# Performance work log

Hardware: AMD Instinct MI355X
Metric: run time of the kernel (lower is better)

The kernel has to match this reference:

```python
import jax, jax.numpy as jnp
import numpy as np

H = 5120       # hidden_size
NH = 128       # num_heads
QLR = 1536     # q_lora_rank
DR = 64        # qk_rope_head_dim
KVLR = 512     # kv_lora_rank
DV = 128       # v_head_dim
DN = 128       # qk_nope_head_dim
DQ = 192       # q_head_dim
THETA = 10000.0
EPS = 1e-6


def _rmsnorm(x, w, eps=EPS):
    xf = x.astype(jnp.float32)
    var = jnp.mean(xf * xf, axis=-1, keepdims=True)
    return (w * (xf * jax.lax.rsqrt(var + eps))).astype(x.dtype)


def _rope(x, cos, sin):
    # Llama-style complex rotation on interleaved pairs along last dim.
    xr = x.reshape(x.shape[:-1] + (-1, 2))
    x0, x1 = xr[..., 0], xr[..., 1]
    out = jnp.stack([x0 * cos - x1 * sin, x0 * sin + x1 * cos], axis=-1)
    return out.reshape(x.shape)


def setup_inputs() -> dict:
    key = jax.random.key(0)
    ks = jax.random.split(key, 8)
    b, kv_len = 2, 2048
    s = 0.02  # scaled-down normal init for numerical sanity (math unchanged)
    return {
        "hidden_states": jax.random.normal(ks[0], (b, 1, H), jnp.float32),
        "compressed_kv_normed_cache": jax.random.normal(ks[1], (b, kv_len, KVLR), jnp.float32),
        "k_pe_cache": jax.random.normal(ks[2], (b, kv_len, DR), jnp.float32),
        "q_a_w": jax.random.normal(ks[3], (QLR, H), jnp.float32) * s,
        "q_a_ln_w": jnp.ones((QLR,), jnp.float32),
        "q_b_w": jax.random.normal(ks[4], (NH * DQ, QLR), jnp.float32) * s,
        "kv_b_w": jax.random.normal(ks[5], (NH * (DN + DV), KVLR), jnp.float32) * s,
        "o_w": jax.random.normal(ks[6], (H, NH * DV), jnp.float32) * s,
    }


def reference(hidden_states, compressed_kv_normed_cache, k_pe_cache,
              q_a_w, q_a_ln_w, q_b_w, kv_b_w, o_w):
    b = hidden_states.shape[0]
    kv_len = k_pe_cache.shape[1]

    # Q path: down-proj -> RMSNorm -> up-proj
    q_a = jnp.einsum('bqh,rh->bqr', hidden_states, q_a_w)          # [b,1,QLR]
    q_a = _rmsnorm(q_a, q_a_ln_w)
    q = jnp.einsum('bqr,or->bqo', q_a, q_b_w).reshape(b, NH, DQ)   # q_len==1
    q_nope, q_pe = q[..., :DN], q[..., DN:]                        # [b,NH,128],[b,NH,64]

    # RoPE tables
    inv_freq = 1.0 / (THETA ** (jnp.arange(0, DR, 2, dtype=jnp.float32) / DR))  # [32]
    ang = jnp.arange(kv_len, dtype=jnp.float32)[:, None] * inv_freq             # [kv_len,32]
    cos, sin = jnp.cos(ang), jnp.sin(ang)

    # query rotated at position kv_len-1 (torch code repeats q then takes last slot)
    q_pe = _rope(q_pe, cos[-1], sin[-1])                           # [b,NH,64]
    k_pe = _rope(k_pe_cache, cos[None], sin[None])                 # [b,kv_len,64]

    # KV decompression (shared latent -> per-head nope-key and value)
    kv = jnp.einsum('bkc,oc->bko', compressed_kv_normed_cache, kv_b_w)
    kv = kv.reshape(b, kv_len, NH, DN + DV)
    k_nope, v = kv[..., :DN], kv[..., DN:]                         # [b,kv,NH,128] each

    # scores: nope part + rope part (k_pe broadcast across heads)
    scores = (jnp.einsum('bhd,bkhd->bhk', q_nope, k_nope)
              + jnp.einsum('bhd,bkd->bhk', q_pe, k_pe)) * (DQ ** -0.5)
    attn = jax.nn.softmax(scores.astype(jnp.float32), axis=-1).astype(hidden_states.dtype)

    out = jnp.einsum('bhk,bkhd->bhd', attn, v).reshape(b, 1, NH * DV)
    return jnp.einsum('bqo,ho->bqh', out, o_w)                     # [b,1,H]
```

## Files before the change

kernel.cpp:

```cpp
#include <hip/hip_runtime.h>
#include <math.h>

constexpr int kH    = 5120;
constexpr int kQLR  = 1536;
constexpr int kNH   = 128;
constexpr int kDQ   = 192;
constexpr int kDN   = 128;
constexpr int kDR   = 64;
constexpr int kKVLR = 512;
constexpr int kDV   = 128;

template<int IN, int SPLIT, bool ATOMIC>
__global__ __launch_bounds__(256) void gemv2_k(const float* __restrict__ W,
                                               const float* __restrict__ x,
                                               float* __restrict__ y, int R) {
  constexpr int CH = IN / SPLIT;
  constexpr int F4 = CH / 256;
  int lane = threadIdx.x & 63, wave = threadIdx.x >> 6;
  int r0 = blockIdx.x * 8 + wave * 2;
  int c0 = blockIdx.y * CH;
  const float4* W0 = (const float4*)(W + (size_t)r0 * IN + c0);
  const float4* W1 = (const float4*)(W + (size_t)(r0 + 1) * IN + c0);
  const float4* x0 = (const float4*)(x + c0);
  const float4* x1 = (const float4*)(x + IN + c0);
  float a00 = 0.f, a01 = 0.f, a10 = 0.f, a11 = 0.f;
#pragma unroll 4
  for (int i = 0; i < F4; ++i) {
    int idx = lane + (i << 6);
    float4 w0 = W0[idx];
    float4 w1 = W1[idx];
    float4 u = x0[idx];
    float4 v = x1[idx];
    a00 = fmaf(w0.x,u.x,fmaf(w0.y,u.y,fmaf(w0.z,u.z,fmaf(w0.w,u.w,a00))));
    a01 = fmaf(w0.x,v.x,fmaf(w0.y,v.y,fmaf(w0.z,v.z,fmaf(w0.w,v.w,a01))));
    a10 = fmaf(w1.x,u.x,fmaf(w1.y,u.y,fmaf(w1.z,u.z,fmaf(w1.w,u.w,a10))));
    a11 = fmaf(w1.x,v.x,fmaf(w1.y,v.y,fmaf(w1.z,v.z,fmaf(w1.w,v.w,a11))));
  }
#pragma unroll
  for (int off = 32; off > 0; off >>= 1) {
    a00 += __shfl_down(a00, off, 64);
    a01 += __shfl_down(a01, off, 64);
    a10 += __shfl_down(a10, off, 64);
    a11 += __shfl_down(a11, off, 64);
  }
  if (lane == 0) {
    if (ATOMIC) {
      atomicAdd(&y[r0], a00);
      atomicAdd(&y[(size_t)R + r0], a01);
      atomicAdd(&y[r0 + 1], a10);
      atomicAdd(&y[(size_t)R + r0 + 1], a11);
    } else {
      y[r0] = a00;
      y[(size_t)R + r0] = a01;
      y[r0 + 1] = a10;
      y[(size_t)R + r0 + 1] = a11;
    }
  }
}

__global__ __launch_bounds__(256) void rmsnorm_k(const float* __restrict__ qa,
                                                 const float* __restrict__ w,
                                                 float* __restrict__ out) {
  int b = blockIdx.x, t = threadIdx.x;
  const float* x = qa + (size_t)b * kQLR;
  float s = 0.f;
  for (int i = t; i < kQLR; i += 256) { float v = x[i]; s = fmaf(v, v, s); }
  __shared__ float red[4];
#pragma unroll
  for (int off = 32; off > 0; off >>= 1) s += __shfl_down(s, off, 64);
  if ((t & 63) == 0) red[t >> 6] = s;
  __syncthreads();
  float tot = red[0] + red[1] + red[2] + red[3];
  float scale = rsqrtf(tot / (float)kQLR + 1e-6f);
  for (int i = t; i < kQLR; i += 256) out[(size_t)b * kQLR + i] = x[i] * scale * w[i];
}

__global__ __launch_bounds__(256) void qabs_k(const float* __restrict__ q,
                                              const float* __restrict__ kvw,
                                              float* __restrict__ qabs) {
  int h = blockIdx.x, ds = blockIdx.y;
  int t = threadIdx.x;
  __shared__ float qn[2][32];
  if (t < 64) {
    int b = t >> 5, d = t & 31;
    qn[b][d] = q[((size_t)b * kNH + h) * kDQ + ds * 32 + d];
  }
  __syncthreads();
  float a0x = 0.f, a0y = 0.f, a1x = 0.f, a1y = 0.f;
  const float* wb = kvw + ((size_t)h * 256 + ds * 32) * kKVLR + t * 2;
#pragma unroll 4
  for (int d = 0; d < 32; ++d) {
    float2 w = *(const float2*)(wb + (size_t)d * kKVLR);
    float q0 = qn[0][d], q1 = qn[1][d];
    a0x = fmaf(q0, w.x, a0x); a0y = fmaf(q0, w.y, a0y);
    a1x = fmaf(q1, w.x, a1x); a1y = fmaf(q1, w.y, a1y);
  }
  float* p0 = qabs + (size_t)h * kKVLR + t * 2;
  float* p1 = qabs + ((size_t)kNH + h) * kKVLR + t * 2;
  atomicAdd(p0, a0x); atomicAdd(p0 + 1, a0y);
  atomicAdd(p1, a1x); atomicAdd(p1 + 1, a1y);
}

__global__ __launch_bounds__(256) void attn_k(const float* __restrict__ qabs,
                                              const float* __restrict__ qfull,
                                              const float* __restrict__ c,
                                              const float* __restrict__ kpe,
                                              float* __restrict__ ctxp,
                                              float* __restrict__ ml, int KV) {
  int ks = blockIdx.x, hg = blockIdx.y, b = blockIdx.z;
  int t = threadIdx.x, lane = t & 63, wave = t >> 6;
  int h0 = __builtin_amdgcn_readfirstlane(hg * 16 + wave * 4);
  int k0 = ks * 64;
  __shared__ float cl[64 * 129];
  __shared__ float kl[64 * 65];
  __shared__ float ql[16 * 64];
  __shared__ float al[64 * 20];

  constexpr float kNegLog = -0.28782313662425572f;

  {
    const float4* src = (const float4*)(kpe + ((size_t)b * KV + k0) * kDR);
#pragma unroll
    for (int i = 0; i < 4; ++i) {
      int idx = t + i * 256;
      int r = idx >> 4, c4 = idx & 15;
      float4 v = src[r * 16 + c4];
      float fk = (float)(k0 + r);
      float inv0 = expf(kNegLog * (float)(c4 * 2));
      float inv1 = expf(kNegLog * (float)(c4 * 2 + 1));
      float s0, c0, s1, c1;
      sincosf(fk * inv0, &s0, &c0);
      sincosf(fk * inv1, &s1, &c1);
      float* d = &kl[r * 65 + (c4 << 2)];
      d[0] = v.x * c0 - v.y * s0;
      d[1] = v.x * s0 + v.y * c0;
      d[2] = v.z * c1 - v.w * s1;
      d[3] = v.z * s1 + v.w * c1;
    }
  }
  {
    float fp = (float)(KV - 1);
    for (int pi = t; pi < 512; pi += 256) {
      int j = pi >> 5, i = pi & 31;
      float inv = expf(kNegLog * (float)i);
      float s, cc;
      sincosf(fp * inv, &s, &cc);
      const float* qp = qfull + ((size_t)b * kNH + hg * 16 + j) * kDQ + kDN + 2 * i;
      float x0 = qp[0], x1 = qp[1];
      ql[j * 64 + 2 * i]     = x0 * cc - x1 * s;
      ql[j * 64 + 2 * i + 1] = x0 * s + x1 * cc;
    }
  }

  float acc[4] = {0.f, 0.f, 0.f, 0.f};
  for (int cch = 0; cch < 4; ++cch) {
    __syncthreads();
    const float* cb = c + ((size_t)b * KV + k0) * kKVLR + cch * 128;
#pragma unroll
    for (int i = 0; i < 8; ++i) {
      int idx = t + i * 256;
      int r = idx >> 5, c4 = idx & 31;
      float4 v = *(const float4*)(cb + (size_t)r * kKVLR + (c4 << 2));
      float* d = &cl[r * 129 + (c4 << 2)];
      d[0] = v.x; d[1] = v.y; d[2] = v.z; d[3] = v.w;
    }
    __syncthreads();
    const float* qb = qabs + ((size_t)b * kNH + h0) * kKVLR + cch * 128;
#pragma unroll 4
    for (int cc2 = 0; cc2 < 128; ++cc2) {
      float cv = cl[lane * 129 + cc2];
#pragma unroll
      for (int j = 0; j < 4; ++j)
        acc[j] = fmaf(cv, qb[(size_t)j * kKVLR + cc2], acc[j]);
    }
  }
  {
#pragma unroll 4
    for (int i = 0; i < 64; ++i) {
      float kv = kl[lane * 65 + i];
#pragma unroll
      for (int j = 0; j < 4; ++j)
        acc[j] = fmaf(kv, ql[(wave * 4 + j) * 64 + i], acc[j]);
    }
  }

  const float scale = 1.0f / sqrtf(192.0f);
  float pj[4], mj[4], lj[4];
#pragma unroll
  for (int j = 0; j < 4; ++j) {
    float s = acc[j] * scale;
    float m = s;
#pragma unroll
    for (int off = 32; off > 0; off >>= 1) m = fmaxf(m, __shfl_xor(m, off, 64));
    float p = __expf(s - m);
    float l = p;
#pragma unroll
    for (int off = 32; off > 0; off >>= 1) l += __shfl_xor(l, off, 64);
    pj[j] = p; mj[j] = m; lj[j] = l;
  }
  *(float4*)&al[lane * 20 + wave * 4] = make_float4(pj[0], pj[1], pj[2], pj[3]);
  if (lane == 0) {
#pragma unroll
    for (int j = 0; j < 4; ++j) {
      float2* mp = (float2*)(ml + (((size_t)b * kNH + h0 + j) * 32 + ks) * 2);
      *mp = make_float2(mj[j], lj[j]);
    }
  }
  __syncthreads();

  float2 accv[16];
#pragma unroll
  for (int j = 0; j < 16; ++j) accv[j] = make_float2(0.f, 0.f);
  const float2* c2 = (const float2*)(c + ((size_t)b * KV + k0) * kKVLR);
#pragma unroll 2
  for (int k = 0; k < 64; ++k) {
    float2 cv = c2[k * (kKVLR / 2) + t];
#pragma unroll
    for (int j4 = 0; j4 < 4; ++j4) {
      float4 av = *(const float4*)&al[k * 20 + j4 * 4];
      accv[j4*4+0].x = fmaf(av.x, cv.x, accv[j4*4+0].x);
      accv[j4*4+0].y = fmaf(av.x, cv.y, accv[j4*4+0].y);
      accv[j4*4+1].x = fmaf(av.y, cv.x, accv[j4*4+1].x);
      accv[j4*4+1].y = fmaf(av.y, cv.y, accv[j4*4+1].y);
      accv[j4*4+2].x = fmaf(av.z, cv.x, accv[j4*4+2].x);
      accv[j4*4+2].y = fmaf(av.z, cv.y, accv[j4*4+2].y);
      accv[j4*4+3].x = fmaf(av.w, cv.x, accv[j4*4+3].x);
      accv[j4*4+3].y = fmaf(av.w, cv.y, accv[j4*4+3].y);
    }
  }
#pragma unroll
  for (int j = 0; j < 16; ++j) {
    float2* dst = (float2*)(ctxp + (((size_t)ks * 2 + b) * kNH + hg * 16 + j) * kKVLR);
    dst[t] = accv[j];
  }
}

__global__ __launch_bounds__(256) void vproj_k(const float* __restrict__ ctxp,
                                               const float* __restrict__ ml,
                                               const float* __restrict__ kvw,
                                               float* __restrict__ oh) {
  int h = blockIdx.x, dq = blockIdx.y;
  int t = threadIdx.x, lane = t & 63, wave = t >> 6;
  __shared__ float cf[2 * kKVLR];
  __shared__ float invl[2];
  {
    int b = t >> 7, g = t & 127;
    const float2* mlb = (const float2*)(ml + ((size_t)b * kNH + h) * 64);
    float M = -1e30f;
#pragma unroll 8
    for (int s = 0; s < 32; ++s) M = fmaxf(M, mlb[s].x);
    float L = 0.f;
    float4 a4 = make_float4(0.f, 0.f, 0.f, 0.f);
#pragma unroll 4
    for (int s = 0; s < 32; ++s) {
      float2 e = mlb[s];
      float w = __expf(e.x - M);
      L = fmaf(w, e.y, L);
      const float4* p = (const float4*)(ctxp + (((size_t)s * 2 + b) * kNH + h) * kKVLR);
      float4 v = p[g];
      a4.x = fmaf(w, v.x, a4.x);
      a4.y = fmaf(w, v.y, a4.y);
      a4.z = fmaf(w, v.z, a4.z);
      a4.w = fmaf(w, v.w, a4.w);
    }
    *(float4*)&cf[b * kKVLR + (g << 2)] = a4;
    if (g == 0) invl[b] = 1.0f / L;
  }
  __syncthreads();
  float cr0[8], cr1[8];
#pragma unroll
  for (int j = 0; j < 8; ++j) {
    cr0[j] = cf[lane * 8 + j];
    cr1[j] = cf[kKVLR + lane * 8 + j];
  }
#pragma unroll
  for (int i = 0; i < 8; ++i) {
    int d = dq * 32 + wave * 8 + i;
    const float4* w4 = (const float4*)(kvw + ((size_t)h * 256 + 128 + d) * kKVLR) + lane * 2;
    float4 wa = w4[0], wb = w4[1];
    float s0 = wa.x * cr0[0] + wa.y * cr0[1] + wa.z * cr0[2] + wa.w * cr0[3]
             + wb.x * cr0[4] + wb.y * cr0[5] + wb.z * cr0[6] + wb.w * cr0[7];
    float s1 = wa.x * cr1[0] + wa.y * cr1[1] + wa.z * cr1[2] + wa.w * cr1[3]
             + wb.x * cr1[4] + wb.y * cr1[5] + wb.z * cr1[6] + wb.w * cr1[7];
#pragma unroll
    for (int off = 32; off > 0; off >>= 1) {
      s0 += __shfl_down(s0, off, 64);
      s1 += __shfl_down(s1, off, 64);
    }
    if (lane == 0) {
      oh[(size_t)h * kDV + d] = s0 * invl[0];
      oh[((size_t)kNH + h) * kDV + d] = s1 * invl[1];
    }
  }
}

extern "C" void kernel_launch(void* const* d_in, const int* in_sizes, int n_in,
                              void* d_out, int out_size, void* d_ws, size_t ws_size,
                              hipStream_t stream) {
  const float* hs   = (const float*)d_in[0];
  const float* ckv  = (const float*)d_in[1];
  const float* kpe  = (const float*)d_in[2];
  const float* qaw  = (const float*)d_in[3];
  const float* qlnw = (const float*)d_in[4];
  const float* qbw  = (const float*)d_in[5];
  const float* kvbw = (const float*)d_in[6];
  const float* ow   = (const float*)d_in[7];
  float* out = (float*)d_out;

  int B  = in_sizes[0] / kH;
  int KV = in_sizes[2] / (B * kDR);

  float* ws   = (float*)d_ws;
  float* qa   = ws;
  float* qabs = qa + (size_t)B * kQLR;
  float* qan  = qabs + (size_t)B * kNH * kKVLR;
  float* q    = qan + (size_t)B * kQLR;
  float* ctxp = q + (size_t)B * kNH * kDQ;
  float* ml   = ctxp + (size_t)32 * B * kNH * kKVLR;
  float* oh   = ml + (size_t)B * kNH * 64;

  hipMemsetAsync(qa, 0, ((size_t)B * kQLR + (size_t)B * kNH * kKVLR) * sizeof(float), stream);
  hipMemsetAsync(out, 0, (size_t)out_size * sizeof(float), stream);

  gemv2_k<kH, 4, true><<<dim3(kQLR / 8, 4), 256, 0, stream>>>(qaw, hs, qa, kQLR);
  rmsnorm_k<<<B, 256, 0, stream>>>(qa, qlnw, qan);
  gemv2_k<kQLR, 1, false><<<dim3((kNH * kDQ) / 8, 1), 256, 0, stream>>>(qbw, qan, q, kNH * kDQ);
  qabs_k<<<dim3(kNH, 4), 256, 0, stream>>>(q, kvbw, qabs);
  attn_k<<<dim3(KV / 64, 8, B), 256, 0, stream>>>(qabs, q, ckv, kpe, ctxp, ml, KV);
  vproj_k<<<dim3(kNH, 4), 256, 0, stream>>>(ctxp, ml, kvbw, oh);
  gemv2_k<kNH * kDV, 4, true><<<dim3(kH / 8, 4), 256, 0, stream>>>(ow, oh, out, kH);
}
```

Before: 662.0 us.

## Split split-KV fold from vproj and drop atomics in q absorption

The q-absorption kernel now has each block reduce over all 128 nope dims for a column chunk and write directly, replacing four-way split atomics and the large workspace memset. The split-KV softmax merge is moved out of vproj into a separate fold kernel. Before, each of the four dq blocks per head recomputed the same 32-partial reduction over ctxp; now it is done once. This adds one kernel launch and an intermediate ctx buffer. The q-absorption grid also shrinks to fewer, smaller blocks, so less parallelism is available there.

```diff
diff --git a/kernel.cpp b/kernel.cpp
--- a/kernel.cpp
+++ b/kernel.cpp
@@ -75,30 +75,30 @@
   for (int i = t; i < kQLR; i += 256) out[(size_t)b * kQLR + i] = x[i] * scale * w[i];
 }
 
-__global__ __launch_bounds__(256) void qabs_k(const float* __restrict__ q,
-                                              const float* __restrict__ kvw,
-                                              float* __restrict__ qabs) {
-  int h = blockIdx.x, ds = blockIdx.y;
+__global__ __launch_bounds__(128) void qabs2_k(const float* __restrict__ q,
+                                               const float* __restrict__ kvw,
+                                               float* __restrict__ qabs) {
+  int h = blockIdx.x, ch = blockIdx.y;
   int t = threadIdx.x;
-  __shared__ float qn[2][32];
-  if (t < 64) {
-    int b = t >> 5, d = t & 31;
-    qn[b][d] = q[((size_t)b * kNH + h) * kDQ + ds * 32 + d];
+  __shared__ float qn[2][128];
+  for (int i = t; i < 256; i += 128) {
+    int b = i >> 7, d = i & 127;
+    qn[b][d] = q[((size_t)b * kNH + h) * kDQ + d];
   }
   __syncthreads();
   float a0x = 0.f, a0y = 0.f, a1x = 0.f, a1y = 0.f;
-  const float* wb = kvw + ((size_t)h * 256 + ds * 32) * kKVLR + t * 2;
-#pragma unroll 4
-  for (int d = 0; d < 32; ++d) {
-    float2 w = *(const float2*)(wb + (size_t)d * kKVLR);
+  const float2* wb = (const float2*)(kvw + (size_t)h * 256 * kKVLR) + ch * 128 + t;
+#pragma unroll 8
+  for (int d = 0; d < 128; ++d) {
+    float2 w = wb[(size_t)d * (kKVLR / 2)];
     float q0 = qn[0][d], q1 = qn[1][d];
     a0x = fmaf(q0, w.x, a0x); a0y = fmaf(q0, w.y, a0y);
     a1x = fmaf(q1, w.x, a1x); a1y = fmaf(q1, w.y, a1y);
   }
-  float* p0 = qabs + (size_t)h * kKVLR + t * 2;
-  float* p1 = qabs + ((size_t)kNH + h) * kKVLR + t * 2;
-  atomicAdd(p0, a0x); atomicAdd(p0 + 1, a0y);
-  atomicAdd(p1, a1x); atomicAdd(p1 + 1, a1y);
+  float2* p0 = (float2*)(qabs + (size_t)h * kKVLR) + ch * 128 + t;
+  float2* p1 = (float2*)(qabs + ((size_t)kNH + h) * kKVLR) + ch * 128 + t;
+  *p0 = make_float2(a0x, a0y);
+  *p1 = make_float2(a1x, a1y);
 }
 
 __global__ __launch_bounds__(256) void attn_k(const float* __restrict__ qabs,
@@ -235,61 +235,60 @@
   }
 }
 
-__global__ __launch_bounds__(256) void vproj_k(const float* __restrict__ ctxp,
-                                               const float* __restrict__ ml,
+__global__ __launch_bounds__(256) void fold_k(const float* __restrict__ ctxp,
+                                              const float* __restrict__ ml,
+                                              float* __restrict__ ctx,
+                                              float* __restrict__ invl) {
+  int h = blockIdx.x, b = blockIdx.y;
+  int t = threadIdx.x;
+  const float2* mlb = (const float2*)(ml + ((size_t)b * kNH + h) * 64);
+  float M = -1e30f;
+#pragma unroll 8
+  for (int s = 0; s < 32; ++s) M = fmaxf(M, mlb[s].x);
+  float L = 0.f;
+  float2 acc = make_float2(0.f, 0.f);
+#pragma unroll 4
+  for (int s = 0; s < 32; ++s) {
+    float2 e = mlb[s];
+    float w = __expf(e.x - M);
+    L = fmaf(w, e.y, L);
+    float2 v = ((const float2*)(ctxp + (((size_t)s * 2 + b) * kNH + h) * kKVLR))[t];
+    acc.x = fmaf(w, v.x, acc.x);
+    acc.y = fmaf(w, v.y, acc.y);
+  }
+  ((float2*)(ctx + ((size_t)b * kNH + h) * kKVLR))[t] = acc;
+  if (t == 0) invl[(size_t)b * kNH + h] = 1.0f / L;
+}
+
+__global__ __launch_bounds__(256) void vproj_k(const float* __restrict__ ctx,
+                                               const float* __restrict__ invl,
                                                const float* __restrict__ kvw,
                                                float* __restrict__ oh) {
   int h = blockIdx.x, dq = blockIdx.y;
   int t = threadIdx.x, lane = t & 63, wave = t >> 6;
-  __shared__ float cf[2 * kKVLR];
-  __shared__ float invl[2];
-  {
-    int b = t >> 7, g = t & 127;
-    const float2* mlb = (const float2*)(ml + ((size_t)b * kNH + h) * 64);
-    float M = -1e30f;
-#pragma unroll 8
-    for (int s = 0; s < 32; ++s) M = fmaxf(M, mlb[s].x);
-    float L = 0.f;
-    float4 a4 = make_float4(0.f, 0.f, 0.f, 0.f);
-#pragma unroll 4
-    for (int s = 0; s < 32; ++s) {
-      float2 e = mlb[s];
-      float w = __expf(e.x - M);
-      L = fmaf(w, e.y, L);
-      const float4* p = (const float4*)(ctxp + (((size_t)s * 2 + b) * kNH + h) * kKVLR);
-      float4 v = p[g];
-      a4.x = fmaf(w, v.x, a4.x);
-      a4.y = fmaf(w, v.y, a4.y);
-      a4.z = fmaf(w, v.z, a4.z);
-      a4.w = fmaf(w, v.w, a4.w);
-    }
-    *(float4*)&cf[b * kKVLR + (g << 2)] = a4;
-    if (g == 0) invl[b] = 1.0f / L;
-  }
-  __syncthreads();
-  float cr0[8], cr1[8];
-#pragma unroll
-  for (int j = 0; j < 8; ++j) {
-    cr0[j] = cf[lane * 8 + j];
-    cr1[j] = cf[kKVLR + lane * 8 + j];
-  }
+  const float4* c0 = (const float4*)(ctx + (size_t)h * kKVLR) + lane * 2;
+  const float4* c1 = (const float4*)(ctx + ((size_t)kNH + h) * kKVLR) + lane * 2;
+  float4 ca = c0[0], cb = c0[1];
+  float4 da = c1[0], db = c1[1];
+  float inv0 = invl[h];
+  float inv1 = invl[kNH + h];
 #pragma unroll
   for (int i = 0; i < 8; ++i) {
     int d = dq * 32 + wave * 8 + i;
     const float4* w4 = (const float4*)(kvw + ((size_t)h * 256 + 128 + d) * kKVLR) + lane * 2;
     float4 wa = w4[0], wb = w4[1];
-    float s0 = wa.x * cr0[0] + wa.y * cr0[1] + wa.z * cr0[2] + wa.w * cr0[3]
-             + wb.x * cr0[4] + wb.y * cr0[5] + wb.z * cr0[6] + wb.w * cr0[7];
-    float s1 = wa.x * cr1[0] + wa.y * cr1[1] + wa.z * cr1[2] + wa.w * cr1[3]
-             + wb.x * cr1[4] + wb.y * cr1[5] + wb.z * cr1[6] + wb.w * cr1[7];
+    float s0 = wa.x * ca.x + wa.y * ca.y + wa.z * ca.z + wa.w * ca.w
+             + wb.x * cb.x + wb.y * cb.y + wb.z * cb.z + wb.w * cb.w;
+    float s1 = wa.x * da.x + wa.y * da.y + wa.z * da.z + wa.w * da.w
+             + wb.x * db.x + wb.y * db.y + wb.z * db.z + wb.w * db.w;
 #pragma unroll
     for (int off = 32; off > 0; off >>= 1) {
       s0 += __shfl_down(s0, off, 64);
       s1 += __shfl_down(s1, off, 64);
     }
     if (lane == 0) {
-      oh[(size_t)h * kDV + d] = s0 * invl[0];
-      oh[((size_t)kNH + h) * kDV + d] = s1 * invl[1];
+      oh[(size_t)h * kDV + d] = s0 * inv0;
+      oh[((size_t)kNH + h) * kDV + d] = s1 * inv1;
     }
   }
 }
@@ -312,21 +311,24 @@
 
   float* ws   = (float*)d_ws;
   float* qa   = ws;
-  float* qabs = qa + (size_t)B * kQLR;
-  float* qan  = qabs + (size_t)B * kNH * kKVLR;
+  float* qan  = qa + (size_t)B * kQLR;
   float* q    = qan + (size_t)B * kQLR;
-  float* ctxp = q + (size_t)B * kNH * kDQ;
+  float* qabs = q + (size_t)B * kNH * kDQ;
+  float* ctxp = qabs + (size_t)B * kNH * kKVLR;
   float* ml   = ctxp + (size_t)32 * B * kNH * kKVLR;
-  float* oh   = ml + (size_t)B * kNH * 64;
-
-  hipMemsetAsync(qa, 0, ((size_t)B * kQLR + (size_t)B * kNH * kKVLR) * sizeof(float), stream);
+  float* ctx  = ml + (size_t)B * kNH * 64;
+  float* invl = ctx + (size_t)B * kNH * kKVLR;
+  float* oh   = invl + (size_t)B * kNH;
+
+  hipMemsetAsync(qa, 0, (size_t)B * kQLR * sizeof(float), stream);
   hipMemsetAsync(out, 0, (size_t)out_size * sizeof(float), stream);
 
   gemv2_k<kH, 4, true><<<dim3(kQLR / 8, 4), 256, 0, stream>>>(qaw, hs, qa, kQLR);
   rmsnorm_k<<<B, 256, 0, stream>>>(qa, qlnw, qan);
   gemv2_k<kQLR, 1, false><<<dim3((kNH * kDQ) / 8, 1), 256, 0, stream>>>(qbw, qan, q, kNH * kDQ);
-  qabs_k<<<dim3(kNH, 4), 256, 0, stream>>>(q, kvbw, qabs);
+  qabs2_k<<<dim3(kNH, 2), 128, 0, stream>>>(q, kvbw, qabs);
   attn_k<<<dim3(KV / 64, 8, B), 256, 0, stream>>>(qabs, q, ckv, kpe, ctxp, ml, KV);
-  vproj_k<<<dim3(kNH, 4), 256, 0, stream>>>(ctxp, ml, kvbw, oh);
+  fold_k<<<dim3(kNH, B), 256, 0, stream>>>(ctxp, ml, ctx, invl);
+  vproj_k<<<dim3(kNH, 4), 256, 0, stream>>>(ctx, invl, kvbw, oh);
   gemv2_k<kNH * kDV, 4, true><<<dim3(kH / 8, 4), 256, 0, stream>>>(ow, oh, out, kH);
 }
```

After: 659.8 us. No clear change (-0.3%).
